# Performance work log

Measured on AMD Instinct MI355X. Metric: run time of the kernel, lower is better.

Reference implementation:

```python
import jax, jax.numpy as jnp
import numpy as np

NUM_HEADS = 16

def setup_inputs() -> dict:
    key = jax.random.key(0)
    ks = jax.random.split(key, 8)
    B, S, D = 2, 2048, 1024
    w = lambda k: jax.random.normal(k, (D, D), dtype=jnp.float32) * 0.02
    return {
        "x": jax.random.normal(ks[0], (B, S, D), dtype=jnp.float32),
        "attn_mask": jnp.zeros((S, S), dtype=jnp.float32),
        "key_padding_mask": jnp.zeros((B, S), dtype=bool),
        "Wq": w(ks[1]), "bq": jnp.zeros((D,), jnp.float32),
        "Wk": w(ks[2]), "bk": jnp.zeros((D,), jnp.float32),
        "Wv": w(ks[3]), "bv": jnp.zeros((D,), jnp.float32),
        "Wg": w(ks[4]), "bg": jnp.full((D,), 0.5, jnp.float32),  # gate_bias_init=0.5
        "Wo": w(ks[5]), "bo": jnp.zeros((D,), jnp.float32),
    }

def reference(x, attn_mask, key_padding_mask, Wq, bq, Wk, bk, Wv, bv, Wg, bg, Wo, bo):
    B, S, D = x.shape
    H = NUM_HEADS
    hd = D // H
    scale = jnp.sqrt(jnp.float32(hd)).astype(x.dtype)

    def split_heads(t):  # (B,S,D) -> (B,H,S,hd)
        return t.reshape(B, S, H, hd).transpose(0, 2, 1, 3)

    q = split_heads(x @ Wq + bq)
    k = split_heads(x @ Wk + bk)
    v = split_heads(x @ Wv + bv)

    scores = jnp.einsum("bhqd,bhkd->bhqk", q, k) / scale
    scores = scores + attn_mask[None, None, :, :]
    scores = jnp.where(key_padding_mask[:, None, None, :], -jnp.inf, scores)

    attn_weights = jax.nn.softmax(scores, axis=-1)          # (B,H,S,S)
    attn_out = jnp.einsum("bhqk,bhkd->bhqd", attn_weights, v)

    gate = jax.nn.sigmoid(x @ Wg + bg)                      # (B,S,D)
    gate = split_heads(gate)                                # (B,H,S,hd)
    attn_out = attn_out * gate

    attn_out = attn_out.transpose(0, 2, 1, 3).reshape(B, S, D)
    output = attn_out @ Wo + bo
    avg_attn = attn_weights.mean(axis=1)                    # (B,S,S)
    return output, avg_attn
```

## Files before the change

kernel.cpp:

```cpp
#include <hip/hip_runtime.h>
#include <hip/hip_bf16.h>

#define LOG2E 1.4426950408889634f

typedef short short8 __attribute__((ext_vector_type(8)));
typedef float floatx4 __attribute__((ext_vector_type(4)));

__device__ __forceinline__ floatx4 mfma16(short8 a, short8 b, floatx4 c) {
    return __builtin_amdgcn_mfma_f32_16x16x32_bf16(a, b, c, 0, 0, 0);
}

__device__ __forceinline__ float fexp2(float x) { return __builtin_amdgcn_exp2f(x); }

__device__ __forceinline__ short f2bf(float f) {
    unsigned u = __builtin_bit_cast(unsigned, f);
    u += 0x7FFFu + ((u >> 16) & 1u);
    return (short)(u >> 16);
}
__device__ __forceinline__ unsigned bfpack(float a, float b) {
    unsigned ua = __builtin_bit_cast(unsigned, a) + 0x8000u;
    unsigned ub = __builtin_bit_cast(unsigned, b) + 0x8000u;
    return __builtin_amdgcn_perm(ub, ua, 0x07060302u);
}
__device__ __forceinline__ float bf2f(short s) {
    unsigned u = ((unsigned)(unsigned short)s) << 16;
    return __builtin_bit_cast(float, u);
}

__device__ __forceinline__ void glds16(const void* g, void* l) {
    __builtin_amdgcn_global_load_lds(
        (const __attribute__((address_space(1))) void*)g,
        (__attribute__((address_space(3))) void*)l, 16, 0, 0);
}

__device__ __forceinline__ short8 cvt8(const float* __restrict__ p) {
    float4 a = *reinterpret_cast<const float4*>(p);
    float4 b = *reinterpret_cast<const float4*>(p + 4);
    short8 r;
    r[0] = f2bf(a.x); r[1] = f2bf(a.y); r[2] = f2bf(a.z); r[3] = f2bf(a.w);
    r[4] = f2bf(b.x); r[5] = f2bf(b.y); r[6] = f2bf(b.z); r[7] = f2bf(b.w);
    return r;
}

__global__ __launch_bounds__(256) void cvt_x_kernel(
    const float* __restrict__ in, short* __restrict__ out, int n8)
{
    int i = blockIdx.x * blockDim.x + threadIdx.x;
    if (i < n8)
        *reinterpret_cast<short8*>(out + (size_t)i * 8) = cvt8(in + (size_t)i * 8);
}

__global__ __launch_bounds__(256) void cvt_wt_kernel(
    const float* __restrict__ W0, const float* __restrict__ W1,
    const float* __restrict__ W2, const float* __restrict__ W3,
    const float* __restrict__ W4, short* __restrict__ Wt)
{
    __shared__ short T[64 * 66];
    const int w = blockIdx.z;
    const float* W = (w == 0) ? W0 : (w == 1) ? W1 : (w == 2) ? W2 : (w == 3) ? W3 : W4;
    short* dst = Wt + (size_t)w * 1024 * 1024;
    const int kb = blockIdx.y * 64, nb = blockIdx.x * 64;
    const int t = threadIdx.x;
    const int r = t >> 2, c4 = (t & 3) * 16;
    *reinterpret_cast<short8*>(T + r * 66 + c4)     = cvt8(W + (size_t)(kb + r) * 1024 + nb + c4);
    *reinterpret_cast<short8*>(T + r * 66 + c4 + 8) = cvt8(W + (size_t)(kb + r) * 1024 + nb + c4 + 8);
    __syncthreads();
    short8 o0, o1;
    #pragma unroll
    for (int j = 0; j < 8; ++j) o0[j] = T[(c4 + j) * 66 + r];
    #pragma unroll
    for (int j = 0; j < 8; ++j) o1[j] = T[(c4 + 8 + j) * 66 + r];
    *reinterpret_cast<short8*>(dst + (size_t)(nb + r) * 1024 + kb + c4)     = o0;
    *reinterpret_cast<short8*>(dst + (size_t)(nb + r) * 1024 + kb + c4 + 8) = o1;
}

__global__ __launch_bounds__(256) void flag_scan(
    const float* __restrict__ amask, const unsigned char* __restrict__ kpm,
    int* __restrict__ flag)
{
    const int i = blockIdx.x * 256 + threadIdx.x;
    const float4* a4 = reinterpret_cast<const float4*>(amask);
    float4 v0 = a4[(size_t)i * 2];
    float4 v1 = a4[(size_t)i * 2 + 1];
    bool nz = (v0.x != 0.f) | (v0.y != 0.f) | (v0.z != 0.f) | (v0.w != 0.f)
            | (v1.x != 0.f) | (v1.y != 0.f) | (v1.z != 0.f) | (v1.w != 0.f);
    if (blockIdx.x == 0) {
        const uint4* k4 = reinterpret_cast<const uint4*>(kpm);
        uint4 kv = k4[threadIdx.x];
        nz |= ((kv.x | kv.y | kv.z | kv.w) != 0u);
    }
    if (__ballot(nz) && ((threadIdx.x & 63) == 0)) atomicOr(flag, 1);
}

__global__ __launch_bounds__(256) void mask_prep(
    const float* __restrict__ amask, const unsigned char* __restrict__ kpm,
    float* __restrict__ Mc, const int* __restrict__ flag)
{
    if (*flag == 0) return;
    const int b = blockIdx.z, q = blockIdx.y;
    const int p0 = threadIdx.x * 8;
    float o[8];
    #pragma unroll
    for (int i = 0; i < 8; ++i) {
        int p = p0 + i;
        int j = (p & ~31) | ((p >> 1) & 15) | ((p & 1) << 4);
        unsigned char kb = kpm[b * 2048 + j];
        float a = amask[(size_t)q * 2048 + j];
        o[i] = a * LOG2E + (kb ? -1.0e30f : 0.f);
    }
    float* dst = Mc + ((size_t)b * 2048 + q) * 2048 + p0;
    *reinterpret_cast<float4*>(dst)     = make_float4(o[0], o[1], o[2], o[3]);
    *reinterpret_cast<float4*>(dst + 4) = make_float4(o[4], o[5], o[6], o[7]);
}

__device__ __forceinline__ void gemm_core256p(
    const short* __restrict__ A, const short* __restrict__ Wt,
    int mbase, int nbase, short* Asm, short* Bsm, floatx4 (&acc)[8][4])
{
    const int tid = threadIdx.x;
    const int lane = tid & 63, wid = tid >> 6;
    const int L15 = lane & 15, g = lane >> 4;
    const int wrow = (wid >> 2) * 128, wcol = (wid & 3) * 64;

    const int rl4 = lane >> 2, c4 = lane & 3;
    const int R0 = wid * 32;
    const short* aG = A  + (size_t)(mbase + R0 + rl4) * 1024 + c4 * 8;
    const short* bG = Wt + (size_t)(nbase + R0 + rl4) * 1024 + c4 * 8;

#define STAGE(t_) do {                                                        \
        const int sl_ = (t_) & 3;                                             \
        glds16(aG + (size_t)(t_) * 32,         Asm + sl_ * 8192 + R0 * 32);   \
        glds16(aG + (size_t)(t_) * 32 + 16384, Asm + sl_ * 8192 + R0 * 32 + 512); \
        glds16(bG + (size_t)(t_) * 32,         Bsm + sl_ * 8192 + R0 * 32);   \
        glds16(bG + (size_t)(t_) * 32 + 16384, Bsm + sl_ * 8192 + R0 * 32 + 512); \
    } while (0)

#define BARRIER_SB() do {                                                     \
        __builtin_amdgcn_sched_barrier(0);                                    \
        __builtin_amdgcn_s_barrier();                                         \
        __builtin_amdgcn_sched_barrier(0);                                    \
    } while (0)

    STAGE(0); STAGE(1);
    asm volatile("s_waitcnt vmcnt(4)" ::: "memory");
    BARRIER_SB();

    for (int t = 0; t < 32; ++t) {
        const int sl = t & 3;
        const short* Ab = Asm + sl * 8192;
        const short* Bb = Bsm + sl * 8192;
        short8 bf[4], af[4];
        #pragma unroll
        for (int nt = 0; nt < 4; ++nt)
            bf[nt] = *reinterpret_cast<const short8*>(Bb + (wcol + nt * 16 + L15) * 32 + g * 8);
        #pragma unroll
        for (int mt = 0; mt < 4; ++mt)
            af[mt] = *reinterpret_cast<const short8*>(Ab + (wrow + mt * 16 + L15) * 32 + g * 8);
        #pragma unroll
        for (int mt = 0; mt < 4; ++mt)
            #pragma unroll
            for (int nt = 0; nt < 4; ++nt)
                acc[mt][nt] = mfma16(af[mt], bf[nt], acc[mt][nt]);

        if (t + 2 < 32) STAGE(t + 2);

        #pragma unroll
        for (int mt = 0; mt < 4; ++mt)
            af[mt] = *reinterpret_cast<const short8*>(Ab + (wrow + 64 + mt * 16 + L15) * 32 + g * 8);
        #pragma unroll
        for (int mt = 0; mt < 4; ++mt)
            #pragma unroll
            for (int nt = 0; nt < 4; ++nt)
                acc[mt + 4][nt] = mfma16(af[mt], bf[nt], acc[mt + 4][nt]);

        if (t + 2 < 32)      asm volatile("s_waitcnt vmcnt(4)" ::: "memory");
        else if (t + 1 < 32) asm volatile("s_waitcnt vmcnt(0)" ::: "memory");
        BARRIER_SB();
    }

#undef STAGE
#undef BARRIER_SB
}

__device__ __forceinline__ void gemm_core(
    const short* __restrict__ A, const short* __restrict__ Wt,
    int mbase, int nbase, short* Asm, short* Bsm, floatx4 (&acc)[4][4])
{
    const int tid = threadIdx.x;
    const int lane = tid & 63, wid = tid >> 6;
    const int L15 = lane & 15, g = lane >> 4;
    const int wm = (wid >> 1) * 64, wn = (wid & 1) * 64;

    const int rowoff = lane >> 3;
    const int choff = ((lane & 7) ^ rowoff) * 8;
    const short* aP = A  + (size_t)(mbase + wid * 32 + rowoff) * 1024 + choff;
    const short* bP = Wt + (size_t)(nbase + wid * 32 + rowoff) * 1024 + choff;
    short* aL = Asm + wid * 2048;
    short* bL = Bsm + wid * 2048;

    const int xb = L15 & 7;
    const int s0 = (g ^ xb) * 8;
    const int s1 = ((g ^ 4) ^ xb) * 8;

    for (int kb = 0; kb < 1024; kb += 64) {
        __syncthreads();
        #pragma unroll
        for (int j = 0; j < 4; ++j) glds16(aP + kb + j * 8192, aL + j * 512);
        #pragma unroll
        for (int j = 0; j < 4; ++j) glds16(bP + kb + j * 8192, bL + j * 512);
        __syncthreads();
        #pragma unroll
        for (int ks = 0; ks < 2; ++ks) {
            const int so = ks ? s1 : s0;
            short8 af[4], bf[4];
            #pragma unroll
            for (int mt = 0; mt < 4; ++mt)
                af[mt] = *reinterpret_cast<const short8*>(Asm + (wm + mt * 16 + L15) * 64 + so);
            #pragma unroll
            for (int nt = 0; nt < 4; ++nt)
                bf[nt] = *reinterpret_cast<const short8*>(Bsm + (wn + nt * 16 + L15) * 64 + so);
            #pragma unroll
            for (int mt = 0; mt < 4; ++mt)
                #pragma unroll
                for (int nt = 0; nt < 4; ++nt)
                    acc[mt][nt] = mfma16(af[mt], bf[nt], acc[mt][nt]);
        }
    }
}

__global__ __launch_bounds__(512) void qkvg_gemm(
    const short* __restrict__ A, const short* __restrict__ Wt5,
    const float* __restrict__ b0, const float* __restrict__ b1,
    const float* __restrict__ b2, const float* __restrict__ b3,
    short* __restrict__ dQ, short* __restrict__ dK,
    short* __restrict__ dV, short* __restrict__ dG)
{
    __shared__ short Asm[4 * 8192];
    __shared__ short Bsm[4 * 8192];

    const int wg = blockIdx.x;
    const int swz = (wg & 7) * 32 + (wg >> 3);
    const int z = swz >> 6;
    const int rem = swz & 63;
    const int mbase = (rem >> 2) * 256, nbase = (rem & 3) * 256;

    floatx4 acc[8][4] = {};
    gemm_core256p(A, Wt5 + (size_t)z * 1048576, mbase, nbase, Asm, Bsm, acc);

    const int lane = threadIdx.x & 63, wid = threadIdx.x >> 6;
    const int L15 = lane & 15, g = lane >> 4;
    const int wrow = (wid >> 2) * 128, wcol = (wid & 3) * 64;
    const float* bz = (z == 0) ? b0 : (z == 1) ? b1 : (z == 2) ? b2 : b3;
    short* dst = (z == 0) ? dQ : (z == 1) ? dK : (z == 2) ? dV : dG;

    float bvv[4];
    #pragma unroll
    for (int nt = 0; nt < 4; ++nt) bvv[nt] = bz[nbase + wcol + nt * 16 + L15];

    if (z <= 1) {
        const float qsc = (z == 0) ? 0.125f * LOG2E : 1.0f;
        #pragma unroll
        for (int mt = 0; mt < 8; ++mt) {
            #pragma unroll
            for (int r = 0; r < 4; ++r) {
                int row = mbase + wrow + mt * 16 + g * 4 + r;
                int bb = row >> 11, s = row & 2047;
                #pragma unroll
                for (int nt = 0; nt < 4; ++nt) {
                    int col = nbase + wcol + nt * 16 + L15;
                    int hh = col >> 6, dh = col & 63;
                    dst[(((size_t)bb * 16 + hh) * 2048 + s) * 64 + dh] =
                        f2bf((acc[mt][nt][r] + bvv[nt]) * qsc);
                }
            }
        }
    } else if (z == 2) {
        #pragma unroll
        for (int nt = 0; nt < 4; ++nt) {
            int col = nbase + wcol + nt * 16 + L15;
            int hh = col >> 6, dh = col & 63;
            #pragma unroll
            for (int mt = 0; mt < 8; ++mt) {
                #pragma unroll
                for (int r = 0; r < 4; ++r) {
                    int row = mbase + wrow + mt * 16 + g * 4 + r;
                    int bb = row >> 11, s = row & 2047;
                    int sp = (s & ~31) | ((s & 15) << 1) | ((s >> 4) & 1);
                    dst[(((size_t)bb * 16 + hh) * 64 + dh) * 2048 + sp] =
                        f2bf(acc[mt][nt][r] + bvv[nt]);
                }
            }
        }
    } else {
        #pragma unroll
        for (int mt = 0; mt < 8; ++mt) {
            #pragma unroll
            for (int r = 0; r < 4; ++r) {
                int row = mbase + wrow + mt * 16 + g * 4 + r;
                #pragma unroll
                for (int nt = 0; nt < 4; ++nt) {
                    int col = nbase + wcol + nt * 16 + L15;
                    float e = fexp2(-(acc[mt][nt][r] + bvv[nt]) * LOG2E);
                    dst[(size_t)row * 1024 + col] = f2bf(__builtin_amdgcn_rcpf(1.0f + e));
                }
            }
        }
    }
}

__global__ __launch_bounds__(256) void out_gemm(
    const short* __restrict__ A, const short* __restrict__ Wt,
    const float* __restrict__ bias, float* __restrict__ out)
{
    __shared__ short Asm[128 * 64];
    __shared__ short Bsm[128 * 64];
    const int mbase = blockIdx.y * 128, nbase = blockIdx.x * 128;
    floatx4 acc[4][4] = {};
    gemm_core(A, Wt, mbase, nbase, Asm, Bsm, acc);

    const int lane = threadIdx.x & 63, wid = threadIdx.x >> 6;
    const int L15 = lane & 15, g = lane >> 4;
    const int wm = (wid >> 1) * 64, wn = (wid & 1) * 64;
    #pragma unroll
    for (int nt = 0; nt < 4; ++nt) {
        int col = nbase + wn + nt * 16 + L15;
        float bv = bias[col];
        #pragma unroll
        for (int mt = 0; mt < 4; ++mt)
            #pragma unroll
            for (int r = 0; r < 4; ++r) {
                int row = mbase + wm + mt * 16 + g * 4 + r;
                out[(size_t)row * 1024 + col] = acc[mt][nt][r] + bv;
            }
    }
}

template<bool MASKED>
__device__ __forceinline__ void flash_body(
    const short* __restrict__ Q, const short* __restrict__ K,
    const short* __restrict__ Vt, const short* __restrict__ G,
    const float* __restrict__ Mc, short* __restrict__ att,
    float* __restrict__ inv_l,
    short* Ksm, short* Vsm, short* Psm)
{
    const int tid = threadIdx.x;
    const int lane = tid & 63, wid = tid >> 6;
    const int L15 = lane & 15, g = lane >> 4;
    const int b = blockIdx.z, h = blockIdx.x;
    const int bh = b * 16 + h;
    const int qb = blockIdx.y * 128 + wid * 32;

    short8 aq0a = *reinterpret_cast<const short8*>(Q + ((size_t)bh * 2048 + qb + L15) * 64 + g * 8);
    short8 aq1a = *reinterpret_cast<const short8*>(Q + ((size_t)bh * 2048 + qb + L15) * 64 + 32 + g * 8);
    short8 aq0b = *reinterpret_cast<const short8*>(Q + ((size_t)bh * 2048 + qb + 16 + L15) * 64 + g * 8);
    short8 aq1b = *reinterpret_cast<const short8*>(Q + ((size_t)bh * 2048 + qb + 16 + L15) * 64 + 32 + g * 8);

    floatx4 Oa[4] = {}, Ob[4] = {};
    float la[4] = {0.f, 0.f, 0.f, 0.f}, lb[4] = {0.f, 0.f, 0.f, 0.f};

    const int krow = lane >> 3;
    const int kch  = ((lane & 7) ^ krow) * 8;
    const bool isK = wid < 2;
    const int sw = isK ? wid : (wid - 2);
    const short* gP;
    if (isK) {
        gP = K + ((size_t)bh * 2048 + sw * 32 + krow) * 64 + kch;
    } else {
        const int vsc = (lane & 7) ^ krow;
        const int vhd = sw * 32 + 2 * krow + (vsc >> 2);
        gP = Vt + ((size_t)bh * 64 + vhd) * 2048 + (vsc & 3) * 8;
    }

    const int x7 = L15 & 7;
    const int sk0 = (g ^ x7) * 8, sk1 = ((g ^ 4) ^ x7) * 8;
    const int sv = (((L15 & 1) * 4 + g) ^ ((L15 >> 1) & 7)) * 8;
    const int vp = (L15 >> 1) * 64;

    short* Pw = Psm + wid * 2304;

    const float* mcPa[4];
    float2 mc0a[4], mc1a[4], mc0b[4], mc1b[4];
    if (MASKED) {
        #pragma unroll
        for (int r = 0; r < 4; ++r) {
            mcPa[r] = Mc + ((size_t)b * 2048 + qb + g * 4 + r) * 2048 + 2 * L15;
            mc0a[r] = *reinterpret_cast<const float2*>(mcPa[r]);
            mc1a[r] = *reinterpret_cast<const float2*>(mcPa[r] + 32);
            mc0b[r] = *reinterpret_cast<const float2*>(mcPa[r] + 16 * 2048);
            mc1b[r] = *reinterpret_cast<const float2*>(mcPa[r] + 16 * 2048 + 32);
        }
    }

    if (isK) {
        #pragma unroll
        for (int j = 0; j < 4; ++j)
            glds16(gP + j * 512, Ksm + sw * 2048 + j * 512);
    } else {
        #pragma unroll
        for (int j = 0; j < 2; ++j) {
            glds16(gP + j * 32768,      Vsm + sw * 1024 + j * 512);
            glds16(gP + j * 32768 + 32, Vsm + 2048 + sw * 1024 + j * 512);
        }
    }

    for (int kb = 0; kb < 2048; kb += 64) {
        const int cur = (kb >> 6) & 1;
        __syncthreads();
        const int nb = kb + 64;
        const bool more = nb < 2048;
        float2 nmc0a[4], nmc1a[4], nmc0b[4], nmc1b[4];
        if (more) {
            const int nbuf = (cur ^ 1) * 4096;
            if (isK) {
                #pragma unroll
                for (int j = 0; j < 4; ++j)
                    glds16(gP + (size_t)nb * 64 + j * 512, Ksm + nbuf + sw * 2048 + j * 512);
            } else {
                #pragma unroll
                for (int j = 0; j < 2; ++j) {
                    glds16(gP + nb + j * 32768,      Vsm + nbuf + sw * 1024 + j * 512);
                    glds16(gP + nb + j * 32768 + 32, Vsm + nbuf + 2048 + sw * 1024 + j * 512);
                }
            }
            if (MASKED) {
                #pragma unroll
                for (int r = 0; r < 4; ++r) {
                    nmc0a[r] = *reinterpret_cast<const float2*>(mcPa[r] + nb);
                    nmc1a[r] = *reinterpret_cast<const float2*>(mcPa[r] + nb + 32);
                    nmc0b[r] = *reinterpret_cast<const float2*>(mcPa[r] + 16 * 2048 + nb);
                    nmc1b[r] = *reinterpret_cast<const float2*>(mcPa[r] + 16 * 2048 + nb + 32);
                }
            }
        }

        const short* Kb = Ksm + cur * 4096;
        floatx4 sa[4], sb[4];
        #pragma unroll
        for (int kt = 0; kt < 4; ++kt) {
            short8 kf0 = *reinterpret_cast<const short8*>(Kb + (kt * 16 + L15) * 64 + sk0);
            short8 kf1 = *reinterpret_cast<const short8*>(Kb + (kt * 16 + L15) * 64 + sk1);
            sa[kt] = {};
            sa[kt] = mfma16(aq0a, kf0, sa[kt]);
            sa[kt] = mfma16(aq1a, kf1, sa[kt]);
            sb[kt] = {};
            sb[kt] = mfma16(aq0b, kf0, sb[kt]);
            sb[kt] = mfma16(aq1b, kf1, sb[kt]);
        }

        #pragma unroll
        for (int r = 0; r < 4; ++r) {
            float e0 = fexp2(MASKED ? sa[0][r] + mc0a[r].x : sa[0][r]);
            float e1 = fexp2(MASKED ? sa[1][r] + mc0a[r].y : sa[1][r]);
            float e2 = fexp2(MASKED ? sa[2][r] + mc1a[r].x : sa[2][r]);
            float e3 = fexp2(MASKED ? sa[3][r] + mc1a[r].y : sa[3][r]);
            la[r] += (e0 + e1) + (e2 + e3);
            *reinterpret_cast<unsigned*>(&Pw[(g * 4 + r) * 72 + 2 * L15])      = bfpack(e0, e1);
            *reinterpret_cast<unsigned*>(&Pw[(g * 4 + r) * 72 + 32 + 2 * L15]) = bfpack(e2, e3);
            float f0 = fexp2(MASKED ? sb[0][r] + mc0b[r].x : sb[0][r]);
            float f1 = fexp2(MASKED ? sb[1][r] + mc0b[r].y : sb[1][r]);
            float f2 = fexp2(MASKED ? sb[2][r] + mc1b[r].x : sb[2][r]);
            float f3 = fexp2(MASKED ? sb[3][r] + mc1b[r].y : sb[3][r]);
            lb[r] += (f0 + f1) + (f2 + f3);
            *reinterpret_cast<unsigned*>(&Pw[(16 + g * 4 + r) * 72 + 2 * L15])      = bfpack(f0, f1);
            *reinterpret_cast<unsigned*>(&Pw[(16 + g * 4 + r) * 72 + 32 + 2 * L15]) = bfpack(f2, f3);
        }
        short8 ap0a = *reinterpret_cast<const short8*>(&Pw[L15 * 72 + g * 8]);
        short8 ap1a = *reinterpret_cast<const short8*>(&Pw[L15 * 72 + 32 + g * 8]);
        short8 ap0b = *reinterpret_cast<const short8*>(&Pw[(16 + L15) * 72 + g * 8]);
        short8 ap1b = *reinterpret_cast<const short8*>(&Pw[(16 + L15) * 72 + 32 + g * 8]);
        const short* Vb0 = Vsm + cur * 4096;
        const short* Vb1 = Vb0 + 2048;
        #pragma unroll
        for (int t = 0; t < 4; ++t) {
            short8 vf0 = *reinterpret_cast<const short8*>(Vb0 + t * 512 + vp + sv);
            short8 vf1 = *reinterpret_cast<const short8*>(Vb1 + t * 512 + vp + sv);
            Oa[t] = mfma16(ap0a, vf0, Oa[t]);
            Oa[t] = mfma16(ap1a, vf1, Oa[t]);
            Ob[t] = mfma16(ap0b, vf0, Ob[t]);
            Ob[t] = mfma16(ap1b, vf1, Ob[t]);
        }

        if (MASKED && more) {
            #pragma unroll
            for (int r = 0; r < 4; ++r) {
                mc0a[r] = nmc0a[r]; mc1a[r] = nmc1a[r];
                mc0b[r] = nmc0b[r]; mc1b[r] = nmc1b[r];
            }
        }
    }

    float inva[4], invb[4];
    #pragma unroll
    for (int r = 0; r < 4; ++r) {
        float ls = la[r];
        ls += __shfl_xor(ls, 1);
        ls += __shfl_xor(ls, 2);
        ls += __shfl_xor(ls, 4);
        ls += __shfl_xor(ls, 8);
        inva[r] = 1.0f / ls;
        if (L15 == 0) inv_l[(size_t)bh * 2048 + qb + g * 4 + r] = inva[r];
        float lt = lb[r];
        lt += __shfl_xor(lt, 1);
        lt += __shfl_xor(lt, 2);
        lt += __shfl_xor(lt, 4);
        lt += __shfl_xor(lt, 8);
        invb[r] = 1.0f / lt;
        if (L15 == 0) inv_l[(size_t)bh * 2048 + qb + 16 + g * 4 + r] = invb[r];
    }
    #pragma unroll
    for (int t = 0; t < 4; ++t) {
        int col = h * 64 + t * 16 + L15;
        #pragma unroll
        for (int r = 0; r < 4; ++r) {
            size_t qra = qb + g * 4 + r;
            float gta = bf2f(G[((size_t)b * 2048 + qra) * 1024 + col]);
            att[((size_t)b * 2048 + qra) * 1024 + col] = f2bf(Oa[t][r] * inva[r] * gta);
            size_t qrb = qb + 16 + g * 4 + r;
            float gtb = bf2f(G[((size_t)b * 2048 + qrb) * 1024 + col]);
            att[((size_t)b * 2048 + qrb) * 1024 + col] = f2bf(Ob[t][r] * invb[r] * gtb);
        }
    }
}

__global__ __launch_bounds__(256, 2) void flash_attn(
    const short* __restrict__ Q, const short* __restrict__ K,
    const short* __restrict__ Vt, const short* __restrict__ G,
    const float* __restrict__ Mc, const int* __restrict__ flag,
    short* __restrict__ att, float* __restrict__ inv_l)
{
    __shared__ short Ksm[2 * 4096];
    __shared__ short Vsm[2 * 4096];
    __shared__ short Psm[4 * 2304];
    if (*flag)
        flash_body<true>(Q, K, Vt, G, Mc, att, inv_l, Ksm, Vsm, Psm);
    else
        flash_body<false>(Q, K, Vt, G, Mc, att, inv_l, Ksm, Vsm, Psm);
}

template<bool MASKED>
__device__ __forceinline__ void avg_body(
    const short* __restrict__ Q, const short* __restrict__ K,
    const float* __restrict__ inv_l, float* mca, short* KsmBase)
{
    const int tid = threadIdx.x;
    const int lane = tid & 63, wid = tid >> 6;
    const int L15 = lane & 15, g = lane >> 4;
    const int b = blockIdx.z;
    const int qb = blockIdx.y * 64 + wid * 16;
    const int ks = blockIdx.x * 128;

    float pm[4][2][4];
    if (MASKED) {
        #pragma unroll
        for (int c = 0; c < 4; ++c)
            #pragma unroll
            for (int r = 0; r < 4; ++r) {
                size_t qr = qb + g * 4 + r;
                float2 m = *reinterpret_cast<const float2*>(
                    mca + ((size_t)b * 2048 + qr) * 2048 + ks + c * 32 + 2 * L15);
                pm[c][0][r] = m.x;
                pm[c][1][r] = m.y;
            }
    }
    float av[4][2][4] = {};

    const int rowoff = lane >> 3;
    const int choff = ((lane & 7) ^ rowoff) * 8;
    const int x7 = L15 & 7;
    const int sk0 = (g ^ x7) * 8, sk1 = ((g ^ 4) ^ x7) * 8;
    short* kL[2] = { KsmBase + wid * 2048, KsmBase + 8192 + wid * 2048 };

    {
        const short* p = K + ((size_t)(b * 16) * 2048 + ks + wid * 32 + rowoff) * 64 + choff;
        #pragma unroll
        for (int j = 0; j < 4; ++j) glds16(p + j * 512, kL[0] + j * 512);
    }
    short8 aq0 = *reinterpret_cast<const short8*>(Q + ((size_t)(b * 16) * 2048 + qb + L15) * 64 + g * 8);
    short8 aq1 = *reinterpret_cast<const short8*>(Q + ((size_t)(b * 16) * 2048 + qb + L15) * 64 + 32 + g * 8);
    float iv[4];
    #pragma unroll
    for (int r = 0; r < 4; ++r) iv[r] = inv_l[(size_t)(b * 16) * 2048 + qb + g * 4 + r];

    for (int h = 0; h < 16; ++h) {
        __syncthreads();
        short8 naq0, naq1;
        float niv[4];
        if (h < 15) {
            int nbh = b * 16 + h + 1;
            const short* p = K + ((size_t)nbh * 2048 + ks + wid * 32 + rowoff) * 64 + choff;
            #pragma unroll
            for (int j = 0; j < 4; ++j) glds16(p + j * 512, kL[(h + 1) & 1] + j * 512);
            naq0 = *reinterpret_cast<const short8*>(Q + ((size_t)nbh * 2048 + qb + L15) * 64 + g * 8);
            naq1 = *reinterpret_cast<const short8*>(Q + ((size_t)nbh * 2048 + qb + L15) * 64 + 32 + g * 8);
            #pragma unroll
            for (int r = 0; r < 4; ++r) niv[r] = inv_l[(size_t)nbh * 2048 + qb + g * 4 + r];
        }

        const short* Kb = KsmBase + (h & 1) * 8192;
        #pragma unroll
        for (int c = 0; c < 4; ++c) {
            const short* kbase = Kb + c * 32 * 64;
            floatx4 s0 = {}, s1 = {};
            s0 = mfma16(aq0, *reinterpret_cast<const short8*>(kbase + L15 * 64 + sk0), s0);
            s0 = mfma16(aq1, *reinterpret_cast<const short8*>(kbase + L15 * 64 + sk1), s0);
            s1 = mfma16(aq0, *reinterpret_cast<const short8*>(kbase + (16 + L15) * 64 + sk0), s1);
            s1 = mfma16(aq1, *reinterpret_cast<const short8*>(kbase + (16 + L15) * 64 + sk1), s1);
            #pragma unroll
            for (int r = 0; r < 4; ++r) {
                av[c][0][r] += fexp2(MASKED ? s0[r] + pm[c][0][r] : s0[r]) * iv[r];
                av[c][1][r] += fexp2(MASKED ? s1[r] + pm[c][1][r] : s1[r]) * iv[r];
            }
        }
        if (h < 15) {
            aq0 = naq0; aq1 = naq1;
            #pragma unroll
            for (int r = 0; r < 4; ++r) iv[r] = niv[r];
        }
    }
    #pragma unroll
    for (int c = 0; c < 4; ++c)
        #pragma unroll
        for (int t = 0; t < 2; ++t)
            #pragma unroll
            for (int r = 0; r < 4; ++r) {
                size_t qr = qb + g * 4 + r;
                int col = ks + c * 32 + t * 16 + L15;
                mca[((size_t)b * 2048 + qr) * 2048 + col] = av[c][t][r] * 0.0625f;
            }
}

__global__ __launch_bounds__(256) void avg_attn_kernel(
    const short* __restrict__ Q, const short* __restrict__ K,
    const float* __restrict__ inv_l, float* mca, const int* __restrict__ flag)
{
    __shared__ short Ksm[2 * 128 * 64];
    if (*flag)
        avg_body<true>(Q, K, inv_l, mca, Ksm);
    else
        avg_body<false>(Q, K, inv_l, mca, Ksm);
}

extern "C" void kernel_launch(void* const* d_in, const int* in_sizes, int n_in,
                              void* d_out, int out_size, void* d_ws, size_t ws_size,
                              hipStream_t stream)
{
    const float* x  = (const float*)d_in[0];
    const float* amask = (const float*)d_in[1];
    const unsigned char* kpm = (const unsigned char*)d_in[2];
    const float* Wq = (const float*)d_in[3];
    const float* bq = (const float*)d_in[4];
    const float* Wk = (const float*)d_in[5];
    const float* bk = (const float*)d_in[6];
    const float* Wv = (const float*)d_in[7];
    const float* bv = (const float*)d_in[8];
    const float* Wg = (const float*)d_in[9];
    const float* bg = (const float*)d_in[10];
    const float* Wo = (const float*)d_in[11];
    const float* bo = (const float*)d_in[12];

    char* ws = (char*)d_ws;
    const size_t MB = 1u << 20;
    short* Xb    = (short*)(ws);
    short* Att   = Xb;
    short* Qw    = (short*)(ws + 8 * MB);
    short* Kw    = (short*)(ws + 16 * MB);
    short* Vt    = (short*)(ws + 24 * MB);
    short* Gw    = (short*)(ws + 32 * MB);
    short* Wt    = (short*)(ws + 40 * MB);
    float* stats = (float*)(ws + 50 * MB);
    int*   flagp = (int*)(ws + 50 * MB + 262144);

    float* outp = (float*)d_out;
    float* avgp = (float*)d_out + 4194304;

    hipMemsetAsync(flagp, 0, sizeof(int), stream);

    flag_scan<<<2048, 256, 0, stream>>>(amask, kpm, flagp);

    cvt_x_kernel<<<2048, 256, 0, stream>>>(x, Xb, 524288);
    cvt_wt_kernel<<<dim3(16, 16, 5), 256, 0, stream>>>(Wq, Wk, Wv, Wg, Wo, Wt);
    mask_prep<<<dim3(1, 2048, 2), 256, 0, stream>>>(amask, kpm, avgp, flagp);

    qkvg_gemm<<<256, 512, 0, stream>>>(Xb, Wt, bq, bk, bv, bg, Qw, Kw, Vt, Gw);

    flash_attn<<<dim3(16, 16, 2), 256, 0, stream>>>(Qw, Kw, Vt, Gw, avgp, flagp, Att, stats);

    avg_attn_kernel<<<dim3(16, 32, 2), 256, 0, stream>>>(Qw, Kw, stats, avgp, flagp);

    out_gemm<<<dim3(8, 32), 256, 0, stream>>>(Att, Wt + 4 * 1048576, bo, outp);
}
```

Baseline: 266.1 us.

## Software-pipeline P·V of previous tile behind QK^T of current tile

Restructures the flash-attention loop so the P·V matmul for the previous key tile runs after the QK^T matmul of the current tile, with a triple-buffered V shared-memory ring to keep the old V tile alive. The goal is to overlap the exp/softmax VALU work and LDS round-trip of P with independent MFMA work, hiding latency within each iteration. A final P·V epilogue handles the last tile. This raises LDS usage (extra 8KB V buffer), which may reduce occupancy at 2 blocks per CU, and adds register pressure from holding the P fragments across the iteration.

```diff
diff --git a/kernel.cpp b/kernel.cpp
--- a/kernel.cpp
+++ b/kernel.cpp
@@ -403,23 +403,34 @@
         }
     }
 
-    for (int kb = 0; kb < 2048; kb += 64) {
-        const int cur = (kb >> 6) & 1;
+    for (int tt = 0; tt < 32; ++tt) {
+        const int kcur = tt & 1;
         __syncthreads();
-        const int nb = kb + 64;
+        const int nb = (tt + 1) * 64;
         const bool more = nb < 2048;
+        const bool havePrev = tt > 0;
+
+        short8 ap0a, ap1a, ap0b, ap1b;
+        if (havePrev) {
+            ap0a = *reinterpret_cast<const short8*>(&Pw[L15 * 72 + g * 8]);
+            ap1a = *reinterpret_cast<const short8*>(&Pw[L15 * 72 + 32 + g * 8]);
+            ap0b = *reinterpret_cast<const short8*>(&Pw[(16 + L15) * 72 + g * 8]);
+            ap1b = *reinterpret_cast<const short8*>(&Pw[(16 + L15) * 72 + 32 + g * 8]);
+        }
+
         float2 nmc0a[4], nmc1a[4], nmc0b[4], nmc1b[4];
         if (more) {
-            const int nbuf = (cur ^ 1) * 4096;
             if (isK) {
+                const int nbufK = ((tt + 1) & 1) * 4096;
                 #pragma unroll
                 for (int j = 0; j < 4; ++j)
-                    glds16(gP + (size_t)nb * 64 + j * 512, Ksm + nbuf + sw * 2048 + j * 512);
+                    glds16(gP + (size_t)nb * 64 + j * 512, Ksm + nbufK + sw * 2048 + j * 512);
             } else {
+                const int nbufV = ((tt + 1) % 3) * 4096;
                 #pragma unroll
                 for (int j = 0; j < 2; ++j) {
-                    glds16(gP + nb + j * 32768,      Vsm + nbuf + sw * 1024 + j * 512);
-                    glds16(gP + nb + j * 32768 + 32, Vsm + nbuf + 2048 + sw * 1024 + j * 512);
+                    glds16(gP + nb + j * 32768,      Vsm + nbufV + sw * 1024 + j * 512);
+                    glds16(gP + nb + j * 32768 + 32, Vsm + nbufV + 2048 + sw * 1024 + j * 512);
                 }
             }
             if (MASKED) {
@@ -433,7 +444,7 @@
             }
         }
 
-        const short* Kb = Ksm + cur * 4096;
+        const short* Kb = Ksm + kcur * 4096;
         floatx4 sa[4], sb[4];
         #pragma unroll
         for (int kt = 0; kt < 4; ++kt) {
@@ -445,6 +456,20 @@
             sb[kt] = {};
             sb[kt] = mfma16(aq0b, kf0, sb[kt]);
             sb[kt] = mfma16(aq1b, kf1, sb[kt]);
+        }
+
+        if (havePrev) {
+            const short* Vb0 = Vsm + ((tt + 2) % 3) * 4096;
+            const short* Vb1 = Vb0 + 2048;
+            #pragma unroll
+            for (int t = 0; t < 4; ++t) {
+                short8 vf0 = *reinterpret_cast<const short8*>(Vb0 + t * 512 + vp + sv);
+                short8 vf1 = *reinterpret_cast<const short8*>(Vb1 + t * 512 + vp + sv);
+                Oa[t] = mfma16(ap0a, vf0, Oa[t]);
+                Oa[t] = mfma16(ap1a, vf1, Oa[t]);
+                Ob[t] = mfma16(ap0b, vf0, Ob[t]);
+                Ob[t] = mfma16(ap1b, vf1, Ob[t]);
+            }
         }
 
         #pragma unroll
@@ -464,11 +489,22 @@
             *reinterpret_cast<unsigned*>(&Pw[(16 + g * 4 + r) * 72 + 2 * L15])      = bfpack(f0, f1);
             *reinterpret_cast<unsigned*>(&Pw[(16 + g * 4 + r) * 72 + 32 + 2 * L15]) = bfpack(f2, f3);
         }
+
+        if (MASKED && more) {
+            #pragma unroll
+            for (int r = 0; r < 4; ++r) {
+                mc0a[r] = nmc0a[r]; mc1a[r] = nmc1a[r];
+                mc0b[r] = nmc0b[r]; mc1b[r] = nmc1b[r];
+            }
+        }
+    }
+
+    {
         short8 ap0a = *reinterpret_cast<const short8*>(&Pw[L15 * 72 + g * 8]);
         short8 ap1a = *reinterpret_cast<const short8*>(&Pw[L15 * 72 + 32 + g * 8]);
         short8 ap0b = *reinterpret_cast<const short8*>(&Pw[(16 + L15) * 72 + g * 8]);
         short8 ap1b = *reinterpret_cast<const short8*>(&Pw[(16 + L15) * 72 + 32 + g * 8]);
-        const short* Vb0 = Vsm + cur * 4096;
+        const short* Vb0 = Vsm + (31 % 3) * 4096;
         const short* Vb1 = Vb0 + 2048;
         #pragma unroll
         for (int t = 0; t < 4; ++t) {
@@ -478,14 +514,6 @@
             Oa[t] = mfma16(ap1a, vf1, Oa[t]);
             Ob[t] = mfma16(ap0b, vf0, Ob[t]);
             Ob[t] = mfma16(ap1b, vf1, Ob[t]);
-        }
-
-        if (MASKED && more) {
-            #pragma unroll
-            for (int r = 0; r < 4; ++r) {
-                mc0a[r] = nmc0a[r]; mc1a[r] = nmc1a[r];
-                mc0b[r] = nmc0b[r]; mc1b[r] = nmc1b[r];
-            }
         }
     }
 
@@ -529,7 +557,7 @@
     short* __restrict__ att, float* __restrict__ inv_l)
 {
     __shared__ short Ksm[2 * 4096];
-    __shared__ short Vsm[2 * 4096];
+    __shared__ short Vsm[3 * 4096];
     __shared__ short Psm[4 * 2304];
     if (*flag)
         flash_body<true>(Q, K, Vt, G, Mc, att, inv_l, Ksm, Vsm, Psm);
```

After: 269.5 us. Within noise of the previous version (+1.3%).

## Pipeline output GEMM with 4-slot LDS ring and async prefetch two stages ahead

Applied to the files above, without the earlier changes.

Replaces the output-projection GEMM core's single-buffered K loop (sync, load 64-wide K tile, sync, compute) with a 4-slot shared-memory ring of 32-wide K tiles. Global-to-LDS loads for stage t+2 are issued mid-compute with counted vmcnt waits and a single barrier per step. The aim is to overlap memory latency with MFMA work and halve the barriers per K step. The trade-offs are more LDS per block and the loss of the previous XOR swizzle, so LDS bank conflicts are possible.

```diff
diff --git a/kernel.cpp b/kernel.cpp
--- a/kernel.cpp
+++ b/kernel.cpp
@@ -182,7 +182,7 @@
 #undef BARRIER_SB
 }
 
-__device__ __forceinline__ void gemm_core(
+__device__ __forceinline__ void gemm_core128p(
     const short* __restrict__ A, const short* __restrict__ Wt,
     int mbase, int nbase, short* Asm, short* Bsm, floatx4 (&acc)[4][4])
 {
@@ -191,41 +191,64 @@
     const int L15 = lane & 15, g = lane >> 4;
     const int wm = (wid >> 1) * 64, wn = (wid & 1) * 64;
 
-    const int rowoff = lane >> 3;
-    const int choff = ((lane & 7) ^ rowoff) * 8;
-    const short* aP = A  + (size_t)(mbase + wid * 32 + rowoff) * 1024 + choff;
-    const short* bP = Wt + (size_t)(nbase + wid * 32 + rowoff) * 1024 + choff;
-    short* aL = Asm + wid * 2048;
-    short* bL = Bsm + wid * 2048;
-
-    const int xb = L15 & 7;
-    const int s0 = (g ^ xb) * 8;
-    const int s1 = ((g ^ 4) ^ xb) * 8;
-
-    for (int kb = 0; kb < 1024; kb += 64) {
-        __syncthreads();
-        #pragma unroll
-        for (int j = 0; j < 4; ++j) glds16(aP + kb + j * 8192, aL + j * 512);
-        #pragma unroll
-        for (int j = 0; j < 4; ++j) glds16(bP + kb + j * 8192, bL + j * 512);
-        __syncthreads();
-        #pragma unroll
-        for (int ks = 0; ks < 2; ++ks) {
-            const int so = ks ? s1 : s0;
-            short8 af[4], bf[4];
-            #pragma unroll
-            for (int mt = 0; mt < 4; ++mt)
-                af[mt] = *reinterpret_cast<const short8*>(Asm + (wm + mt * 16 + L15) * 64 + so);
+    const int rl4 = lane >> 2, c4 = lane & 3;
+    const int R0 = wid * 32;
+    const short* aG = A  + (size_t)(mbase + R0 + rl4) * 1024 + c4 * 8;
+    const short* bG = Wt + (size_t)(nbase + R0 + rl4) * 1024 + c4 * 8;
+
+#define STAGE(t_) do {                                                        \
+        const int sl_ = (t_) & 3;                                             \
+        glds16(aG + (size_t)(t_) * 32,         Asm + sl_ * 4096 + R0 * 32);   \
+        glds16(aG + (size_t)(t_) * 32 + 16384, Asm + sl_ * 4096 + R0 * 32 + 512); \
+        glds16(bG + (size_t)(t_) * 32,         Bsm + sl_ * 4096 + R0 * 32);   \
+        glds16(bG + (size_t)(t_) * 32 + 16384, Bsm + sl_ * 4096 + R0 * 32 + 512); \
+    } while (0)
+
+#define BARRIER_SB() do {                                                     \
+        __builtin_amdgcn_sched_barrier(0);                                    \
+        __builtin_amdgcn_s_barrier();                                         \
+        __builtin_amdgcn_sched_barrier(0);                                    \
+    } while (0)
+
+    STAGE(0); STAGE(1);
+    asm volatile("s_waitcnt vmcnt(4)" ::: "memory");
+    BARRIER_SB();
+
+    for (int t = 0; t < 32; ++t) {
+        const int sl = t & 3;
+        const short* Ab = Asm + sl * 4096;
+        const short* Bb = Bsm + sl * 4096;
+        short8 bf[4], af[2];
+        #pragma unroll
+        for (int nt = 0; nt < 4; ++nt)
+            bf[nt] = *reinterpret_cast<const short8*>(Bb + (wn + nt * 16 + L15) * 32 + g * 8);
+        #pragma unroll
+        for (int mt = 0; mt < 2; ++mt)
+            af[mt] = *reinterpret_cast<const short8*>(Ab + (wm + mt * 16 + L15) * 32 + g * 8);
+        #pragma unroll
+        for (int mt = 0; mt < 2; ++mt)
             #pragma unroll
             for (int nt = 0; nt < 4; ++nt)
-                bf[nt] = *reinterpret_cast<const short8*>(Bsm + (wn + nt * 16 + L15) * 64 + so);
-            #pragma unroll
-            for (int mt = 0; mt < 4; ++mt)
-                #pragma unroll
-                for (int nt = 0; nt < 4; ++nt)
-                    acc[mt][nt] = mfma16(af[mt], bf[nt], acc[mt][nt]);
-        }
-    }
+                acc[mt][nt] = mfma16(af[mt], bf[nt], acc[mt][nt]);
+
+        if (t + 2 < 32) STAGE(t + 2);
+
+        #pragma unroll
+        for (int mt = 0; mt < 2; ++mt)
+            af[mt] = *reinterpret_cast<const short8*>(Ab + (wm + 32 + mt * 16 + L15) * 32 + g * 8);
+        #pragma unroll
+        for (int mt = 0; mt < 2; ++mt)
+            #pragma unroll
+            for (int nt = 0; nt < 4; ++nt)
+                acc[mt + 2][nt] = mfma16(af[mt], bf[nt], acc[mt + 2][nt]);
+
+        if (t + 2 < 32)      asm volatile("s_waitcnt vmcnt(4)" ::: "memory");
+        else if (t + 1 < 32) asm volatile("s_waitcnt vmcnt(0)" ::: "memory");
+        BARRIER_SB();
+    }
+
+#undef STAGE
+#undef BARRIER_SB
 }
 
 __global__ __launch_bounds__(512) void qkvg_gemm(
@@ -312,11 +335,11 @@
     const short* __restrict__ A, const short* __restrict__ Wt,
     const float* __restrict__ bias, float* __restrict__ out)
 {
-    __shared__ short Asm[128 * 64];
-    __shared__ short Bsm[128 * 64];
+    __shared__ short Asm[4 * 4096];
+    __shared__ short Bsm[4 * 4096];
     const int mbase = blockIdx.y * 128, nbase = blockIdx.x * 128;
     floatx4 acc[4][4] = {};
-    gemm_core(A, Wt, mbase, nbase, Asm, Bsm, acc);
+    gemm_core128p(A, Wt, mbase, nbase, Asm, Bsm, acc);
 
     const int lane = threadIdx.x & 63, wid = threadIdx.x >> 6;
     const int L15 = lane & 15, g = lane >> 4;
```

Result: slower. 276.0 us (+3.7%).
